# Kernel optimization log

Hardware: AMD Instinct MI355X
Metric: run time of the kernel (lower is better)

The kernel has to match this reference:

```python
import math
import jax, jax.numpy as jnp
import numpy as np

HEADS = 9
EMBED = 32
TEMPERATURE = 3000.0

def _conv1x1(x, W, b):
    # x: [B,C,H,W], W: [O,C], b: [O]  (1x1 conv == channel matmul)
    return jnp.einsum('bchw,oc->bohw', x, W) + b[None, :, None, None]

def setup_inputs() -> dict:
    key = jax.random.key(0)
    ks = jax.random.split(key, 14)
    B, H, W = 2, 64, 64
    h2, w2 = 32, 32
    hd = HEADS * EMBED  # 288
    s = 0.1
    return {
        'second_frame': jax.random.normal(ks[0], (B, 3, H, W), jnp.float32),
        'first_frame_aligned': jax.random.normal(ks[1], (B, 3, H, W), jnp.float32),
        'second_frame_feat': jax.random.normal(ks[2], (B, 4, h2, w2), jnp.float32),
        'first_frame_feat_aligned': jax.random.normal(ks[3], (B, 4, h2, w2), jnp.float32),
        'Wq': jax.random.normal(ks[4], (hd, 3), jnp.float32) * s,
        'bq': jax.random.normal(ks[5], (hd,), jnp.float32) * s,
        'Wk': jax.random.normal(ks[6], (hd, 3), jnp.float32) * s,
        'bk': jax.random.normal(ks[7], (hd,), jnp.float32) * s,
        'Wv': jax.random.normal(ks[8], (hd, 4), jnp.float32) * s,
        'bv': jax.random.normal(ks[9], (hd,), jnp.float32) * s,
        'Wp': jax.random.normal(ks[10], (4, hd), jnp.float32) * s,
        'bp': jax.random.normal(ks[11], (4,), jnp.float32) * s,
        'Wt': jax.random.normal(ks[12], (1, EMBED), jnp.float32) * s,
        'bt': jax.random.normal(ks[13], (1,), jnp.float32) * s,
    }

def reference(second_frame, first_frame_aligned, second_frame_feat,
              first_frame_feat_aligned, Wq, bq, Wk, bk, Wv, bv, Wp, bp, Wt, bt):
    B, _, H, W = second_frame.shape
    HW = H * W
    # bilinear upsample of aligned features to (H, W); half-pixel centers == align_corners=False
    feat_up = jax.image.resize(first_frame_feat_aligned,
                               (B, first_frame_feat_aligned.shape[1], H, W),
                               method='linear', antialias=False)
    Q = _conv1x1(second_frame, Wq, bq).reshape(B, HEADS, EMBED, HW)
    K = _conv1x1(first_frame_aligned, Wk, bk).reshape(B, HEADS, EMBED, HW)
    V = _conv1x1(feat_up, Wv, bv).reshape(B, HEADS, EMBED, HW)
    Qn = jnp.transpose(Q, (0, 1, 3, 2))                      # [B,h,HW,d]
    sim = jnp.einsum('bhnd,bhdm->bhnm', Qn, K) / math.sqrt(EMBED)  # [B,h,HW,HW]
    # learned per-query threshold from Q
    t = jnp.einsum('bhnd,od->bhno', Qn, Wt) + bt             # [B,h,HW,1]
    attn = jax.nn.relu((sim - t) / TEMPERATURE)              # no row normalization
    out = jnp.einsum('bhnm,bhdm->bhnd', attn, V)             # [B,h,HW,d]
    out = jnp.transpose(out, (0, 1, 3, 2)).reshape(B, HEADS * EMBED, H, W)
    out_feat = _conv1x1(out, Wp, bp)                         # [B,4,H,W]
    h2, w2 = second_frame_feat.shape[-2:]
    out_feat_down = jax.image.resize(out_feat, (B, out_feat.shape[1], h2, w2),
                                     method='linear', antialias=False)
    final_feat = second_frame_feat + out_feat_down
    return final_feat, out_feat_down
```

## Files before the change

kernel.cpp:

```cpp
#include <hip/hip_runtime.h>
#include <hip/hip_bf16.h>
#include <cstddef>

#define NHEADS 9
#define D 32
#define SQ 4096
#define ZSPLIT 4
#define MBLK (SQ / ZSPLIT)
#define CHUNKS (MBLK / 64)
#define KROW 40
#define VROW 68

typedef __attribute__((ext_vector_type(8))) short bf16x8;
typedef __attribute__((ext_vector_type(4))) short bf16x4;
typedef __attribute__((ext_vector_type(4))) float f32x4;

__device__ __forceinline__ unsigned int f2bf(float f) {
    unsigned int u = __float_as_uint(f);
    u += 0x7fffu + ((u >> 16) & 1u);
    return u >> 16;
}

__global__ __launch_bounds__(256) void prep_kernel(
    const float* __restrict__ x2, const float* __restrict__ x1,
    const float* __restrict__ feat1,
    const float* __restrict__ Wq, const float* __restrict__ bq,
    const float* __restrict__ Wk, const float* __restrict__ bk,
    const float* __restrict__ Wv, const float* __restrict__ bv,
    const float* __restrict__ Wt, const float* __restrict__ bt,
    unsigned short* __restrict__ Qb, unsigned short* __restrict__ Kb,
    unsigned short* __restrict__ Vb, float* __restrict__ tbuf)
{
    int idx = blockIdx.x * blockDim.x + threadIdx.x;
    int g  = idx & 3;
    int n  = (idx >> 2) & (SQ - 1);
    int bh = idx >> 14;
    int h  = bh % NHEADS;
    int b  = bh / NHEADS;

    float xs0 = x2[((size_t)b * 3 + 0) * SQ + n];
    float xs1 = x2[((size_t)b * 3 + 1) * SQ + n];
    float xs2 = x2[((size_t)b * 3 + 2) * SQ + n];
    float ys0 = x1[((size_t)b * 3 + 0) * SQ + n];
    float ys1 = x1[((size_t)b * 3 + 1) * SQ + n];
    float ys2 = x1[((size_t)b * 3 + 2) * SQ + n];

    int yy = n >> 6, xx = n & 63;
    int jy = yy >> 1, jx = xx >> 1;
    int j0, j1, i0, i1; float wy0, wy1, wx0, wx1;
    if (yy & 1) { j0 = jy; j1 = (jy < 31) ? jy + 1 : 31; wy0 = 0.75f; wy1 = 0.25f; }
    else        { j0 = (jy > 0) ? jy - 1 : 0; j1 = jy;   wy0 = 0.25f; wy1 = 0.75f; }
    if (xx & 1) { i0 = jx; i1 = (jx < 31) ? jx + 1 : 31; wx0 = 0.75f; wx1 = 0.25f; }
    else        { i0 = (jx > 0) ? jx - 1 : 0; i1 = jx;   wx0 = 0.25f; wx1 = 0.75f; }

    float fu[4];
#pragma unroll
    for (int c = 0; c < 4; ++c) {
        const float* f = feat1 + ((size_t)b * 4 + c) * 1024;
        fu[c] = wy0 * (wx0 * f[j0 * 32 + i0] + wx1 * f[j0 * 32 + i1]) +
                wy1 * (wx0 * f[j1 * 32 + i0] + wx1 * f[j1 * 32 + i1]);
    }

    const int d0 = g * 8;
    unsigned int qp[4], kp[4], vp[4];
    float tpart = 0.0f;
#pragma unroll
    for (int j = 0; j < 8; ++j) {
        int d = d0 + j, hd = h * D + d;
        float q = bq[hd] + Wq[hd * 3] * xs0 + Wq[hd * 3 + 1] * xs1 + Wq[hd * 3 + 2] * xs2;
        float k = bk[hd] + Wk[hd * 3] * ys0 + Wk[hd * 3 + 1] * ys1 + Wk[hd * 3 + 2] * ys2;
        float v = bv[hd] + Wv[hd * 4] * fu[0] + Wv[hd * 4 + 1] * fu[1] +
                  Wv[hd * 4 + 2] * fu[2] + Wv[hd * 4 + 3] * fu[3];
        tpart += q * Wt[d];
        unsigned int qb_ = f2bf(q), kb_ = f2bf(k), vb_ = f2bf(v);
        if (j & 1) { qp[j >> 1] |= qb_ << 16; kp[j >> 1] |= kb_ << 16; vp[j >> 1] |= vb_ << 16; }
        else       { qp[j >> 1]  = qb_;       kp[j >> 1]  = kb_;       vp[j >> 1]  = vb_; }
    }
    tpart += __shfl_xor(tpart, 1);
    tpart += __shfl_xor(tpart, 2);
    if (g == 0) tbuf[(size_t)bh * SQ + n] = tpart + bt[0];

    size_t base = ((size_t)bh * SQ + n) * D + d0;
    *(uint4*)(Qb + base) = make_uint4(qp[0], qp[1], qp[2], qp[3]);
    *(uint4*)(Kb + base) = make_uint4(kp[0], kp[1], kp[2], kp[3]);
    *(uint4*)(Vb + base) = make_uint4(vp[0], vp[1], vp[2], vp[3]);
}

__global__ __launch_bounds__(256, 6) void attn_kernel(
    const unsigned short* __restrict__ Qb,
    const unsigned short* __restrict__ Kb,
    const unsigned short* __restrict__ Vb,
    const float* __restrict__ tbuf,
    const float* __restrict__ Wp,
    float* __restrict__ of)
{
    __shared__ __align__(16) unsigned short Ks[64 * KROW];
    __shared__ __align__(16) unsigned short Vs[32 * VROW];

    const int bh   = blockIdx.y;
    const int h    = bh % NHEADS;
    const int b    = bh / NHEADS;
    const int n0   = blockIdx.x * 128;
    const int mc0  = blockIdx.z * MBLK;
    const int tid  = threadIdx.x;
    const int wave = tid >> 6;
    const int lane = tid & 63;
    const int l15  = lane & 15;
    const int quad = lane >> 4;

    const int nw1 = n0 + wave * 32;
    const int nw2 = nw1 + 16;

    bf16x8 qf1 = *(const bf16x8*)(Qb + ((size_t)bh * SQ + nw1 + l15) * D + quad * 8);
    bf16x8 qf2 = *(const bf16x8*)(Qb + ((size_t)bh * SQ + nw2 + l15) * D + quad * 8);
    const float tt1 = tbuf[(size_t)bh * SQ + nw1 + l15] * (1.0f / 3000.0f);
    const float tt2 = tbuf[(size_t)bh * SQ + nw2 + l15] * (1.0f / 3000.0f);
    const float s1 = 5.892556509887896e-05f;

    const uint4* Kg4 = (const uint4*)(Kb + (size_t)bh * SQ * D);
    const uint4* Vg4 = (const uint4*)(Vb + (size_t)bh * SQ * D);

    const int krow = tid >> 2;
    const int kcol = (tid & 3) * 8;
    unsigned short* kdst = Ks + krow * KROW + kcol;
    unsigned short* vdst = Vs + kcol * VROW + krow;

    f32x4 acc1l = {0.f,0.f,0.f,0.f}, acc1h = {0.f,0.f,0.f,0.f};
    f32x4 acc2l = {0.f,0.f,0.f,0.f}, acc2h = {0.f,0.f,0.f,0.f};
    const f32x4 z = {0.f,0.f,0.f,0.f};

    uint4 kreg = Kg4[(size_t)mc0 * 4 + tid];
    uint4 vreg = Vg4[(size_t)mc0 * 4 + tid];

    for (int c = 0; c < CHUNKS; ++c) {
        __syncthreads();
        *(uint4*)kdst = kreg;
        {
            union { uint4 u; unsigned short s[8]; } vv; vv.u = vreg;
#pragma unroll
            for (int j = 0; j < 8; ++j) vdst[j * VROW] = vv.s[j];
        }
        kreg = Kg4[(size_t)(mc0 + (c + 1) * 64) * 4 + tid];
        vreg = Vg4[(size_t)(mc0 + (c + 1) * 64) * 4 + tid];
        __syncthreads();

#pragma unroll
        for (int s = 0; s < 4; ++s) {
            bf16x8 kf = *(const bf16x8*)(Ks + (s * 16 + l15) * KROW + quad * 8);
            f32x4 st1 = __builtin_amdgcn_mfma_f32_16x16x32_bf16(kf, qf1, z, 0, 0, 0);
            f32x4 st2 = __builtin_amdgcn_mfma_f32_16x16x32_bf16(kf, qf2, z, 0, 0, 0);
            bf16x4 va = *(const bf16x4*)(Vs + l15 * VROW + s * 16 + quad * 4);
            bf16x4 vb = *(const bf16x4*)(Vs + (l15 + 16) * VROW + s * 16 + quad * 4);

            float a0 = fmaxf(fmaf(st1[0], s1, -tt1), 0.0f);
            float a1 = fmaxf(fmaf(st1[1], s1, -tt1), 0.0f);
            float a2 = fmaxf(fmaf(st1[2], s1, -tt1), 0.0f);
            float a3 = fmaxf(fmaf(st1[3], s1, -tt1), 0.0f);
            union { __hip_bfloat162 h2[2]; bf16x4 v; } p1;
            p1.h2[0] = __float22bfloat162_rn(make_float2(a0, a1));
            p1.h2[1] = __float22bfloat162_rn(make_float2(a2, a3));

            float b0 = fmaxf(fmaf(st2[0], s1, -tt2), 0.0f);
            float b1 = fmaxf(fmaf(st2[1], s1, -tt2), 0.0f);
            float b2 = fmaxf(fmaf(st2[2], s1, -tt2), 0.0f);
            float b3 = fmaxf(fmaf(st2[3], s1, -tt2), 0.0f);
            union { __hip_bfloat162 h2[2]; bf16x4 v; } p2;
            p2.h2[0] = __float22bfloat162_rn(make_float2(b0, b1));
            p2.h2[1] = __float22bfloat162_rn(make_float2(b2, b3));

            acc1l = __builtin_amdgcn_mfma_f32_16x16x16bf16_1k(va, p1.v, acc1l, 0, 0, 0);
            acc1h = __builtin_amdgcn_mfma_f32_16x16x16bf16_1k(vb, p1.v, acc1h, 0, 0, 0);
            acc2l = __builtin_amdgcn_mfma_f32_16x16x16bf16_1k(va, p2.v, acc2l, 0, 0, 0);
            acc2h = __builtin_amdgcn_mfma_f32_16x16x16bf16_1k(vb, p2.v, acc2h, 0, 0, 0);
        }
    }

    const float* wph = Wp + h * D + quad * 4;
#pragma unroll
    for (int o = 0; o < 4; ++o) {
        float c1 = 0.0f, c2 = 0.0f;
#pragma unroll
        for (int r = 0; r < 4; ++r) {
            c1 += acc1l[r] * wph[o * 288 + r] + acc1h[r] * wph[o * 288 + 16 + r];
            c2 += acc2l[r] * wph[o * 288 + r] + acc2h[r] * wph[o * 288 + 16 + r];
        }
        c1 += __shfl_xor(c1, 16); c1 += __shfl_xor(c1, 32);
        c2 += __shfl_xor(c2, 16); c2 += __shfl_xor(c2, 32);
        if (quad == 0) {
            atomicAdd(&of[((size_t)b * 4 + o) * SQ + nw1 + l15], c1);
            atomicAdd(&of[((size_t)b * 4 + o) * SQ + nw2 + l15], c2);
        }
    }
}

__global__ void final_kernel(const float* __restrict__ of,
                             const float* __restrict__ sff,
                             const float* __restrict__ bp,
                             float* __restrict__ dout)
{
    int tid = blockIdx.x * blockDim.x + threadIdx.x;
    if (tid >= 8192) return;
    int i  = tid & 31;
    int jj = (tid >> 5) & 31;
    int bo = tid >> 10;
    int o  = bo & 3;
    const float* src = of + (size_t)bo * SQ;
    int y = jj * 2, x = i * 2;
    float dval = 0.25f * (src[y * 64 + x] + src[y * 64 + x + 1] +
                          src[(y + 1) * 64 + x] + src[(y + 1) * 64 + x + 1]) + bp[o];
    dout[tid]        = sff[tid] + dval;
    dout[8192 + tid] = dval;
}

extern "C" void kernel_launch(void* const* d_in, const int* in_sizes, int n_in,
                              void* d_out, int out_size, void* d_ws, size_t ws_size,
                              hipStream_t stream)
{
    const float* second_frame = (const float*)d_in[0];
    const float* first_frame  = (const float*)d_in[1];
    const float* sff          = (const float*)d_in[2];
    const float* ffa          = (const float*)d_in[3];
    const float* Wq = (const float*)d_in[4];
    const float* bq = (const float*)d_in[5];
    const float* Wk = (const float*)d_in[6];
    const float* bk = (const float*)d_in[7];
    const float* Wv = (const float*)d_in[8];
    const float* bv = (const float*)d_in[9];
    const float* Wp = (const float*)d_in[10];
    const float* bp = (const float*)d_in[11];
    const float* Wt = (const float*)d_in[12];
    const float* bt = (const float*)d_in[13];
    float* out = (float*)d_out;

    char* ws = (char*)d_ws;
    const size_t QKV = (size_t)2 * NHEADS * SQ * D * sizeof(unsigned short);
    unsigned short* Qb = (unsigned short*)ws;
    unsigned short* Kb = (unsigned short*)(ws + QKV);
    unsigned short* Vb = (unsigned short*)(ws + 2 * QKV);
    float* tbuf = (float*)(ws + 3 * QKV);
    float* of   = (float*)(ws + 3 * QKV + (size_t)2 * NHEADS * SQ * sizeof(float));

    hipMemsetAsync(of, 0, (size_t)2 * 4 * SQ * sizeof(float), stream);
    prep_kernel<<<1152, 256, 0, stream>>>(second_frame, first_frame, ffa,
                                          Wq, bq, Wk, bk, Wv, bv, Wt, bt,
                                          Qb, Kb, Vb, tbuf);
    dim3 ag(32, 18, ZSPLIT);
    attn_kernel<<<ag, 256, 0, stream>>>(Qb, Kb, Vb, tbuf, Wp, of);
    final_kernel<<<32, 256, 0, stream>>>(of, sff, bp, out);
}
```

Baseline: 149.6 us.

## Widen attention tile to 64 queries per wave and fold scaling into MFMA

```diff
diff --git a/kernel.cpp b/kernel.cpp
--- a/kernel.cpp
+++ b/kernel.cpp
@@ -9,7 +9,7 @@
 #define MBLK (SQ / ZSPLIT)
 #define CHUNKS (MBLK / 64)
 #define KROW 40
-#define VROW 68
+#define VROW 70
 
 typedef __attribute__((ext_vector_type(8))) short bf16x8;
 typedef __attribute__((ext_vector_type(4))) short bf16x4;
@@ -19,6 +19,28 @@
     unsigned int u = __float_as_uint(f);
     u += 0x7fffu + ((u >> 16) & 1u);
     return u >> 16;
+}
+
+__device__ __forceinline__ unsigned int cvt_pk_bf16(float a, float b) {
+#if __has_builtin(__builtin_amdgcn_cvt_pk_bf16_f32)
+    typedef __attribute__((ext_vector_type(2))) __bf16 bf2;
+    union { bf2 v; unsigned int u; } cv;
+    cv.v = __builtin_amdgcn_cvt_pk_bf16_f32(a, b);
+    return cv.u;
+#else
+    return (f2bf(b) << 16) | f2bf(a);
+#endif
+}
+
+__device__ __forceinline__ bf16x4 relu_pack(f32x4 st) {
+    float a0 = fmaxf(st[0], 0.0f);
+    float a1 = fmaxf(st[1], 0.0f);
+    float a2 = fmaxf(st[2], 0.0f);
+    float a3 = fmaxf(st[3], 0.0f);
+    union { unsigned int u[2]; bf16x4 v; } r;
+    r.u[0] = cvt_pk_bf16(a0, a1);
+    r.u[1] = cvt_pk_bf16(a2, a3);
+    return r.v;
 }
 
 __global__ __launch_bounds__(256) void prep_kernel(
@@ -29,9 +51,11 @@
     const float* __restrict__ Wv, const float* __restrict__ bv,
     const float* __restrict__ Wt, const float* __restrict__ bt,
     unsigned short* __restrict__ Qb, unsigned short* __restrict__ Kb,
-    unsigned short* __restrict__ Vb, float* __restrict__ tbuf)
+    unsigned short* __restrict__ Vb, float* __restrict__ tbuf,
+    float* __restrict__ of)
 {
     int idx = blockIdx.x * blockDim.x + threadIdx.x;
+    if (idx < 2 * 4 * SQ) of[idx] = 0.0f;
     int g  = idx & 3;
     int n  = (idx >> 2) & (SQ - 1);
     int bh = idx >> 14;
@@ -86,7 +110,7 @@
     *(uint4*)(Vb + base) = make_uint4(vp[0], vp[1], vp[2], vp[3]);
 }
 
-__global__ __launch_bounds__(256, 6) void attn_kernel(
+__global__ __launch_bounds__(256, 4) void attn_kernel(
     const unsigned short* __restrict__ Qb,
     const unsigned short* __restrict__ Kb,
     const unsigned short* __restrict__ Vb,
@@ -100,7 +124,7 @@
     const int bh   = blockIdx.y;
     const int h    = bh % NHEADS;
     const int b    = bh / NHEADS;
-    const int n0   = blockIdx.x * 128;
+    const int n0   = blockIdx.x * 256;
     const int mc0  = blockIdx.z * MBLK;
     const int tid  = threadIdx.x;
     const int wave = tid >> 6;
@@ -108,14 +132,24 @@
     const int l15  = lane & 15;
     const int quad = lane >> 4;
 
-    const int nw1 = n0 + wave * 32;
-    const int nw2 = nw1 + 16;
-
-    bf16x8 qf1 = *(const bf16x8*)(Qb + ((size_t)bh * SQ + nw1 + l15) * D + quad * 8);
-    bf16x8 qf2 = *(const bf16x8*)(Qb + ((size_t)bh * SQ + nw2 + l15) * D + quad * 8);
-    const float tt1 = tbuf[(size_t)bh * SQ + nw1 + l15] * (1.0f / 3000.0f);
-    const float tt2 = tbuf[(size_t)bh * SQ + nw2 + l15] * (1.0f / 3000.0f);
-    const float s1 = 5.892556509887896e-05f;
+    const int nw = n0 + wave * 64;
+
+    const unsigned short* qbase = Qb + ((size_t)bh * SQ + nw + l15) * D + quad * 8;
+    bf16x8 qfA = *(const bf16x8*)(qbase);
+    bf16x8 qfB = *(const bf16x8*)(qbase + 16 * D);
+    bf16x8 qfC = *(const bf16x8*)(qbase + 32 * D);
+    bf16x8 qfD = *(const bf16x8*)(qbase + 48 * D);
+
+    const float SQRT32 = 5.656854249492381f;
+    const float* tb = tbuf + (size_t)bh * SQ + nw + l15;
+    float TA = tb[0]  * SQRT32;
+    float TB = tb[16] * SQRT32;
+    float TC = tb[32] * SQRT32;
+    float TD = tb[48] * SQRT32;
+    const f32x4 ciA = {-TA, -TA, -TA, -TA};
+    const f32x4 ciB = {-TB, -TB, -TB, -TB};
+    const f32x4 ciC = {-TC, -TC, -TC, -TC};
+    const f32x4 ciD = {-TD, -TD, -TD, -TD};
 
     const uint4* Kg4 = (const uint4*)(Kb + (size_t)bh * SQ * D);
     const uint4* Vg4 = (const uint4*)(Vb + (size_t)bh * SQ * D);
@@ -125,9 +159,10 @@
     unsigned short* kdst = Ks + krow * KROW + kcol;
     unsigned short* vdst = Vs + kcol * VROW + krow;
 
-    f32x4 acc1l = {0.f,0.f,0.f,0.f}, acc1h = {0.f,0.f,0.f,0.f};
-    f32x4 acc2l = {0.f,0.f,0.f,0.f}, acc2h = {0.f,0.f,0.f,0.f};
-    const f32x4 z = {0.f,0.f,0.f,0.f};
+    f32x4 accAl = {0.f,0.f,0.f,0.f}, accAh = {0.f,0.f,0.f,0.f};
+    f32x4 accBl = {0.f,0.f,0.f,0.f}, accBh = {0.f,0.f,0.f,0.f};
+    f32x4 accCl = {0.f,0.f,0.f,0.f}, accCh = {0.f,0.f,0.f,0.f};
+    f32x4 accDl = {0.f,0.f,0.f,0.f}, accDh = {0.f,0.f,0.f,0.f};
 
     uint4 kreg = Kg4[(size_t)mc0 * 4 + tid];
     uint4 vreg = Vg4[(size_t)mc0 * 4 + tid];
@@ -147,48 +182,53 @@
 #pragma unroll
         for (int s = 0; s < 4; ++s) {
             bf16x8 kf = *(const bf16x8*)(Ks + (s * 16 + l15) * KROW + quad * 8);
-            f32x4 st1 = __builtin_amdgcn_mfma_f32_16x16x32_bf16(kf, qf1, z, 0, 0, 0);
-            f32x4 st2 = __builtin_amdgcn_mfma_f32_16x16x32_bf16(kf, qf2, z, 0, 0, 0);
             bf16x4 va = *(const bf16x4*)(Vs + l15 * VROW + s * 16 + quad * 4);
             bf16x4 vb = *(const bf16x4*)(Vs + (l15 + 16) * VROW + s * 16 + quad * 4);
 
-            float a0 = fmaxf(fmaf(st1[0], s1, -tt1), 0.0f);
-            float a1 = fmaxf(fmaf(st1[1], s1, -tt1), 0.0f);
-            float a2 = fmaxf(fmaf(st1[2], s1, -tt1), 0.0f);
-            float a3 = fmaxf(fmaf(st1[3], s1, -tt1), 0.0f);
-            union { __hip_bfloat162 h2[2]; bf16x4 v; } p1;
-            p1.h2[0] = __float22bfloat162_rn(make_float2(a0, a1));
-            p1.h2[1] = __float22bfloat162_rn(make_float2(a2, a3));
-
-            float b0 = fmaxf(fmaf(st2[0], s1, -tt2), 0.0f);
-            float b1 = fmaxf(fmaf(st2[1], s1, -tt2), 0.0f);
-            float b2 = fmaxf(fmaf(st2[2], s1, -tt2), 0.0f);
-            float b3 = fmaxf(fmaf(st2[3], s1, -tt2), 0.0f);
-            union { __hip_bfloat162 h2[2]; bf16x4 v; } p2;
-            p2.h2[0] = __float22bfloat162_rn(make_float2(b0, b1));
-            p2.h2[1] = __float22bfloat162_rn(make_float2(b2, b3));
-
-            acc1l = __builtin_amdgcn_mfma_f32_16x16x16bf16_1k(va, p1.v, acc1l, 0, 0, 0);
-            acc1h = __builtin_amdgcn_mfma_f32_16x16x16bf16_1k(vb, p1.v, acc1h, 0, 0, 0);
-            acc2l = __builtin_amdgcn_mfma_f32_16x16x16bf16_1k(va, p2.v, acc2l, 0, 0, 0);
-            acc2h = __builtin_amdgcn_mfma_f32_16x16x16bf16_1k(vb, p2.v, acc2h, 0, 0, 0);
-        }
-    }
-
+            f32x4 stA = __builtin_amdgcn_mfma_f32_16x16x32_bf16(kf, qfA, ciA, 0, 0, 0);
+            f32x4 stB = __builtin_amdgcn_mfma_f32_16x16x32_bf16(kf, qfB, ciB, 0, 0, 0);
+            f32x4 stC = __builtin_amdgcn_mfma_f32_16x16x32_bf16(kf, qfC, ciC, 0, 0, 0);
+            f32x4 stD = __builtin_amdgcn_mfma_f32_16x16x32_bf16(kf, qfD, ciD, 0, 0, 0);
+
+            bf16x4 pA = relu_pack(stA);
+            bf16x4 pB = relu_pack(stB);
+            bf16x4 pC = relu_pack(stC);
+            bf16x4 pD = relu_pack(stD);
+
+            accAl = __builtin_amdgcn_mfma_f32_16x16x16bf16_1k(va, pA, accAl, 0, 0, 0);
+            accAh = __builtin_amdgcn_mfma_f32_16x16x16bf16_1k(vb, pA, accAh, 0, 0, 0);
+            accBl = __builtin_amdgcn_mfma_f32_16x16x16bf16_1k(va, pB, accBl, 0, 0, 0);
+            accBh = __builtin_amdgcn_mfma_f32_16x16x16bf16_1k(vb, pB, accBh, 0, 0, 0);
+            accCl = __builtin_amdgcn_mfma_f32_16x16x16bf16_1k(va, pC, accCl, 0, 0, 0);
+            accCh = __builtin_amdgcn_mfma_f32_16x16x16bf16_1k(vb, pC, accCh, 0, 0, 0);
+            accDl = __builtin_amdgcn_mfma_f32_16x16x16bf16_1k(va, pD, accDl, 0, 0, 0);
+            accDh = __builtin_amdgcn_mfma_f32_16x16x16bf16_1k(vb, pD, accDh, 0, 0, 0);
+        }
+    }
+
+    const float s1 = 5.892556509887896e-05f;
     const float* wph = Wp + h * D + quad * 4;
 #pragma unroll
     for (int o = 0; o < 4; ++o) {
-        float c1 = 0.0f, c2 = 0.0f;
+        float cA = 0.f, cB = 0.f, cC = 0.f, cD = 0.f;
 #pragma unroll
         for (int r = 0; r < 4; ++r) {
-            c1 += acc1l[r] * wph[o * 288 + r] + acc1h[r] * wph[o * 288 + 16 + r];
-            c2 += acc2l[r] * wph[o * 288 + r] + acc2h[r] * wph[o * 288 + 16 + r];
-        }
-        c1 += __shfl_xor(c1, 16); c1 += __shfl_xor(c1, 32);
-        c2 += __shfl_xor(c2, 16); c2 += __shfl_xor(c2, 32);
+            float wlo = wph[o * 288 + r], whi = wph[o * 288 + 16 + r];
+            cA += accAl[r] * wlo + accAh[r] * whi;
+            cB += accBl[r] * wlo + accBh[r] * whi;
+            cC += accCl[r] * wlo + accCh[r] * whi;
+            cD += accDl[r] * wlo + accDh[r] * whi;
+        }
+        cA += __shfl_xor(cA, 16); cA += __shfl_xor(cA, 32);
+        cB += __shfl_xor(cB, 16); cB += __shfl_xor(cB, 32);
+        cC += __shfl_xor(cC, 16); cC += __shfl_xor(cC, 32);
+        cD += __shfl_xor(cD, 16); cD += __shfl_xor(cD, 32);
         if (quad == 0) {
-            atomicAdd(&of[((size_t)b * 4 + o) * SQ + nw1 + l15], c1);
-            atomicAdd(&of[((size_t)b * 4 + o) * SQ + nw2 + l15], c2);
+            float* ob = &of[((size_t)b * 4 + o) * SQ + nw + l15];
+            atomicAdd(ob,      cA * s1);
+            atomicAdd(ob + 16, cB * s1);
+            atomicAdd(ob + 32, cC * s1);
+            atomicAdd(ob + 48, cD * s1);
         }
     }
 }
@@ -240,11 +280,10 @@
     float* tbuf = (float*)(ws + 3 * QKV);
     float* of   = (float*)(ws + 3 * QKV + (size_t)2 * NHEADS * SQ * sizeof(float));
 
-    hipMemsetAsync(of, 0, (size_t)2 * 4 * SQ * sizeof(float), stream);
     prep_kernel<<<1152, 256, 0, stream>>>(second_frame, first_frame, ffa,
                                           Wq, bq, Wk, bk, Wv, bv, Wt, bt,
-                                          Qb, Kb, Vb, tbuf);
-    dim3 ag(32, 18, ZSPLIT);
+                                          Qb, Kb, Vb, tbuf, of);
+    dim3 ag(16, 18, ZSPLIT);
     attn_kernel<<<ag, 256, 0, stream>>>(Qb, Kb, Vb, tbuf, Wp, of);
     final_kernel<<<32, 256, 0, stream>>>(of, sff, bp, out);
 }
```

Result: slower. 166.4 us (+11.2%).
